# Kernel tuning notes

Hardware: AMD Instinct MI355X
Metric: run time of the kernel (lower is better)

## Reference

```python
import jax, jax.numpy as jnp
import numpy as np

N = 50000          # nodes in homogeneous graph
E_RAND = 450000    # non-self edges
R = 5              # 4 relations + identity
C = 2              # num_channels
L = 2              # num_layers
IN_DIM = 256
HID = 128
NUM_CLASS = 16
N_CAT = 10000


def setup_inputs() -> dict:
    key = jax.random.key(0)
    ks = jax.random.split(key, 10)
    h = jax.random.normal(ks[0], (N, IN_DIM), dtype=jnp.float32)
    src_r = jax.random.randint(ks[1], (E_RAND,), 0, N, dtype=jnp.int32)
    dst_r = jax.random.randint(ks[2], (E_RAND,), 0, N, dtype=jnp.int32)
    et_r = jax.random.randint(ks[3], (E_RAND,), 0, R - 1, dtype=jnp.int32)
    self_idx = jnp.arange(N, dtype=jnp.int32)
    src = jnp.concatenate([src_r, self_idx])
    dst = jnp.concatenate([dst_r, self_idx])
    etype = jnp.concatenate([et_r, jnp.full((N,), R - 1, dtype=jnp.int32)])
    category_idx = jax.random.randint(ks[4], (N_CAT,), 0, N, dtype=jnp.int32)
    # learned params
    gt_w = 0.01 * jax.random.normal(ks[5], (L, C, R), dtype=jnp.float32)
    Wc = jax.random.normal(ks[6], (C, IN_DIM, HID), dtype=jnp.float32) / np.sqrt(IN_DIM)
    W1 = jax.random.normal(ks[7], (C * HID, HID), dtype=jnp.float32) / np.sqrt(C * HID)
    b1 = jnp.zeros((HID,), dtype=jnp.float32)
    W2 = jax.random.normal(ks[8], (HID, NUM_CLASS), dtype=jnp.float32) / np.sqrt(HID)
    b2 = jnp.zeros((NUM_CLASS,), dtype=jnp.float32)
    return {"h": h, "src": src, "dst": dst, "etype": etype,
            "category_idx": category_idx, "gt_w": gt_w, "Wc": Wc,
            "W1": W1, "b1": b1, "W2": W2, "b2": b2}


def reference(h, src, dst, etype, category_idx, gt_w, Wc, W1, b1, W2, b2):
    n = h.shape[0]
    # per-channel input projection: H[c] = h @ Wc[c]  -> [C, N, HID]
    H = jnp.einsum('nd,cdh->cnh', h, Wc)
    seg = lambda v: jax.ops.segment_sum(v, dst, num_segments=n)
    for l in range(gt_w.shape[0]):
        # GTConv: per-channel softmax over relations; summed weighted adjacency
        Filt = jax.nn.softmax(gt_w[l], axis=1)        # [C, R]
        w = Filt[:, etype]                            # [C, E] edge weights
        # EdgeWeightNorm('right'): divide by weighted in-degree of dst
        deg = jax.vmap(seg)(w)                        # [C, N]
        wn = w / deg[:, dst]                          # [C, E]
        # GCNConv: sum_{e: dst=v} H[src(e)] * wn(e)
        msg = H[:, src, :] * wn[:, :, None]           # [C, E, HID]
        H = jax.vmap(seg)(msg)                        # [C, N, HID]
    # concat channels along feature dim (torch.cat(H, dim=1))
    X = jnp.transpose(H, (1, 0, 2)).reshape(n, -1)    # [N, C*HID]
    X = jax.nn.relu(X @ W1 + b1)
    y = X @ W2 + b2
    return y[category_idx]
```

## Files before the change

kernel.cpp:

```cpp
#include <hip/hip_runtime.h>
#include <hip/hip_bf16.h>

#define IN_DIM 256
#define HID 128
#define CCH 2
#define RR 5
#define LL 2
#define NCLS 16

typedef __attribute__((ext_vector_type(8))) short short8;
typedef __attribute__((ext_vector_type(4))) short short4_;
typedef __attribute__((ext_vector_type(4))) float floatx4;

__device__ __forceinline__ unsigned short f2bf(float f) {
    unsigned int u = __float_as_uint(f);
    unsigned int r = (u + 0x7FFFu + ((u >> 16) & 1u)) >> 16;
    return (unsigned short)r;
}

__global__ void cvt_weights(const float* __restrict__ Wc, const float* __restrict__ W1,
                            const float* __restrict__ gt_w,
                            unsigned short* __restrict__ WcT, unsigned short* __restrict__ W1T,
                            float* __restrict__ filt) {
    int i = blockIdx.x * 256 + threadIdx.x;
    if (blockIdx.x == 0 && threadIdx.x < LL * CCH) {
        const float* g = gt_w + threadIdx.x * RR;
        float m = -1e30f;
        for (int r = 0; r < RR; ++r) m = fmaxf(m, g[r]);
        float e[RR], s = 0.f;
        for (int r = 0; r < RR; ++r) { e[r] = __expf(g[r] - m); s += e[r]; }
        for (int r = 0; r < RR; ++r) filt[threadIdx.x * RR + r] = e[r] / s;
    }
    if (i < CCH * HID * IN_DIM) {
        int c = i >> 15;
        int rem = i & 32767;
        int d = rem >> 8;
        int k = rem & 255;
        WcT[i] = f2bf(Wc[((size_t)c * IN_DIM + k) * HID + d]);
    }
    if (i < HID * IN_DIM) {
        int d = i >> 8;
        int k = i & 255;
        W1T[i] = f2bf(W1[(size_t)k * HID + d]);
    }
}

__global__ __launch_bounds__(256, 2) void proj_mfma(const float* __restrict__ h,
                                                    const unsigned short* __restrict__ WcT,
                                                    unsigned short* __restrict__ H0, int N) {
    __shared__ unsigned short Bl[64 * 256];
    int t = threadIdx.x;
    int wv = t >> 6, l = t & 63;
    int l15 = l & 15, lq = l >> 4;
    int n0 = blockIdx.x * 64;

#pragma unroll
    for (int i = 0; i < 16; ++i) {
        int fi = t * 4 + i * 1024;
        int r = fi >> 8;
        int k = fi & 255;
        int node = n0 + r;
        const float* src = h + (size_t)(node < N ? node : N - 1) * IN_DIM + k;
        floatx4 f = *(const floatx4*)src;
        short4_ s4;
        s4[0] = (short)f2bf(f[0]); s4[1] = (short)f2bf(f[1]);
        s4[2] = (short)f2bf(f[2]); s4[3] = (short)f2bf(f[3]);
        int c = k >> 3;
        int half = (k >> 2) & 1;
        int cs = c ^ ((r & 7) << 2);
        *(short4_*)(&Bl[r * 256 + cs * 8 + half * 4]) = s4;
    }
    __syncthreads();

    floatx4 acc[4][4];
#pragma unroll
    for (int m = 0; m < 4; ++m)
#pragma unroll
        for (int n = 0; n < 4; ++n) acc[m][n] = (floatx4){0.f, 0.f, 0.f, 0.f};

#pragma unroll
    for (int kh = 0; kh < 2; ++kh) {
        short8 a[4][4];
#pragma unroll
        for (int mt0 = 0; mt0 < 4; ++mt0) {
            const unsigned short* arow = WcT + (size_t)((wv * 4 + mt0) * 16 + l15) * IN_DIM;
#pragma unroll
            for (int kk = 0; kk < 4; ++kk)
                a[mt0][kk] = *(const short8*)(arow + (kh * 4 + kk) * 32 + lq * 8);
        }
#pragma unroll
        for (int nf = 0; nf < 4; ++nf) {
            int r = nf * 16 + l15;
            short8 b[4];
#pragma unroll
            for (int kk = 0; kk < 4; ++kk) {
                int c = (kh * 4 + kk) * 4 + lq;
                int cs = c ^ ((r & 7) << 2);
                b[kk] = *(const short8*)(&Bl[r * 256 + cs * 8]);
            }
#pragma unroll
            for (int mt0 = 0; mt0 < 4; ++mt0)
#pragma unroll
                for (int kk = 0; kk < 4; ++kk)
                    acc[mt0][nf] = __builtin_amdgcn_mfma_f32_16x16x32_bf16(a[mt0][kk], b[kk],
                                                                           acc[mt0][nf], 0, 0, 0);
        }
    }

#pragma unroll
    for (int mt0 = 0; mt0 < 4; ++mt0) {
        int m0 = (wv * 4 + mt0) * 16 + lq * 4;
#pragma unroll
        for (int nf = 0; nf < 4; ++nf) {
            int node = n0 + nf * 16 + l15;
            if (node < N) {
                short4_ st;
                st[0] = (short)f2bf(acc[mt0][nf][0]); st[1] = (short)f2bf(acc[mt0][nf][1]);
                st[2] = (short)f2bf(acc[mt0][nf][2]); st[3] = (short)f2bf(acc[mt0][nf][3]);
                *(short4_*)(H0 + (size_t)node * (CCH * HID) + m0) = st;
            }
        }
    }
}

__global__ void count_kernel(const int* __restrict__ dst, int* __restrict__ counts, int E) {
    for (int e = blockIdx.x * blockDim.x + threadIdx.x; e < E; e += gridDim.x * blockDim.x)
        atomicAdd(&counts[dst[e]], 1);
}

__global__ void scanA_kernel(const int* __restrict__ counts, int* __restrict__ partials, int n) {
    __shared__ int s[256];
    int t = threadIdx.x;
    int i = blockIdx.x * 256 + t;
    int v = (i < n) ? counts[i] : 0;
    s[t] = v;
    __syncthreads();
    for (int off = 1; off < 256; off <<= 1) {
        int tv = (t >= off) ? s[t - off] : 0;
        __syncthreads();
        s[t] += tv;
        __syncthreads();
    }
    if (t == 255) partials[blockIdx.x] = s[255];
}

__global__ void scanB_kernel(const int* __restrict__ partials, int* __restrict__ chunk_off, int nchunk) {
    __shared__ int s[256];
    int t = threadIdx.x;
    int v = (t < nchunk) ? partials[t] : 0;
    s[t] = v;
    __syncthreads();
    for (int off = 1; off < 256; off <<= 1) {
        int tv = (t >= off) ? s[t - off] : 0;
        __syncthreads();
        s[t] += tv;
        __syncthreads();
    }
    if (t < nchunk) chunk_off[t] = s[t] - v;
}

__global__ void scanC_kernel(const int* __restrict__ counts, const int* __restrict__ chunk_off,
                             int* __restrict__ offsets, int* __restrict__ cursor, int n) {
    __shared__ int s[256];
    int t = threadIdx.x;
    int i = blockIdx.x * 256 + t;
    int v = (i < n) ? counts[i] : 0;
    s[t] = v;
    __syncthreads();
    for (int off = 1; off < 256; off <<= 1) {
        int tv = (t >= off) ? s[t - off] : 0;
        __syncthreads();
        s[t] += tv;
        __syncthreads();
    }
    if (i < n) {
        int incl = chunk_off[blockIdx.x] + s[t];
        offsets[i + 1] = incl;
        cursor[i] = incl - v;
    }
    if (i == 0) offsets[0] = 0;
}

__global__ void fill_kernel(const int* __restrict__ src, const int* __restrict__ dst,
                            const int* __restrict__ etype, int* __restrict__ cursor,
                            int2* __restrict__ epack, int E) {
    for (int e = blockIdx.x * blockDim.x + threadIdx.x; e < E; e += gridDim.x * blockDim.x) {
        int d = dst[e];
        int p = atomicAdd(&cursor[d], 1);
        epack[p] = make_int2(src[e], etype[e]);
    }
}

__global__ __launch_bounds__(256) void agg_kernel(const uint4* __restrict__ Hin,
                                                  uint4* __restrict__ Hout,
                                                  const int* __restrict__ offs,
                                                  const int2* __restrict__ epack,
                                                  const float* __restrict__ filt, int N) {
    int node = blockIdx.x;
    int t = threadIdx.x;
    int g = t >> 5;
    int lane32 = t & 31;
    int c = lane32 >> 4;
    float f0 = filt[c * RR + 0], f1 = filt[c * RR + 1], f2 = filt[c * RR + 2];
    float f3 = filt[c * RR + 3], f4 = filt[c * RR + 4];

    int e0 = offs[node], e1 = offs[node + 1];
    float acc[8];
#pragma unroll
    for (int r = 0; r < 8; ++r) acc[r] = 0.f;
    float deg = 0.f;

    for (int j = e0 + g; j < e1; j += 8) {
        int2 pc = epack[j];
        uint4 v = Hin[(size_t)pc.x * 32 + lane32];
        int et = pc.y;
        float w = (et == 0) ? f0 : (et == 1) ? f1 : (et == 2) ? f2 : (et == 3) ? f3 : f4;
        deg += w;
        acc[0] += w * __uint_as_float(v.x << 16);
        acc[1] += w * __uint_as_float(v.x & 0xFFFF0000u);
        acc[2] += w * __uint_as_float(v.y << 16);
        acc[3] += w * __uint_as_float(v.y & 0xFFFF0000u);
        acc[4] += w * __uint_as_float(v.z << 16);
        acc[5] += w * __uint_as_float(v.z & 0xFFFF0000u);
        acc[6] += w * __uint_as_float(v.w << 16);
        acc[7] += w * __uint_as_float(v.w & 0xFFFF0000u);
    }

#pragma unroll
    for (int r = 0; r < 8; ++r) acc[r] += __shfl_xor(acc[r], 32);
    deg += __shfl_xor(deg, 32);

    __shared__ float sacc[3][8][33];
    __shared__ float sdeg[3][33];
    int wv = t >> 6;
    bool lowhalf = (t & 63) < 32;
    if (wv > 0 && lowhalf) {
#pragma unroll
        for (int r = 0; r < 8; ++r) sacc[wv - 1][r][lane32] = acc[r];
        sdeg[wv - 1][lane32] = deg;
    }
    __syncthreads();
    if (wv == 0 && lowhalf) {
#pragma unroll
        for (int k = 0; k < 3; ++k) {
#pragma unroll
            for (int r = 0; r < 8; ++r) acc[r] += sacc[k][r][lane32];
            deg += sdeg[k][lane32];
        }
        float inv = 1.f / deg;
        uint4 o;
        o.x = (unsigned int)f2bf(acc[0] * inv) | ((unsigned int)f2bf(acc[1] * inv) << 16);
        o.y = (unsigned int)f2bf(acc[2] * inv) | ((unsigned int)f2bf(acc[3] * inv) << 16);
        o.z = (unsigned int)f2bf(acc[4] * inv) | ((unsigned int)f2bf(acc[5] * inv) << 16);
        o.w = (unsigned int)f2bf(acc[6] * inv) | ((unsigned int)f2bf(acc[7] * inv) << 16);
        Hout[(size_t)node * 32 + lane32] = o;
    }
}

__global__ __launch_bounds__(256) void mlp1_mfma(const unsigned short* __restrict__ H2,
                                                 const int* __restrict__ cat,
                                                 const unsigned short* __restrict__ W1T,
                                                 const float* __restrict__ b1,
                                                 float* __restrict__ hidden, int NCAT) {
    int t = threadIdx.x;
    int wv = t >> 6, l = t & 63;
    int l15 = l & 15, lq = l >> 4;
    int i = blockIdx.x * 64 + wv * 16 + l15;
    int iclamp = i < NCAT ? i : NCAT - 1;
    int node = cat[iclamp];

    short8 bfrag[8];
    const unsigned short* xrow = H2 + (size_t)node * (CCH * HID);
#pragma unroll
    for (int kk = 0; kk < 8; ++kk)
        bfrag[kk] = *(const short8*)(xrow + kk * 32 + lq * 8);

#pragma unroll
    for (int mt = 0; mt < 8; ++mt) {
        floatx4 acc = {0.f, 0.f, 0.f, 0.f};
        const unsigned short* arow = W1T + (size_t)(mt * 16 + l15) * (CCH * HID);
#pragma unroll
        for (int kk = 0; kk < 8; ++kk) {
            short8 a = *(const short8*)(arow + kk * 32 + lq * 8);
            acc = __builtin_amdgcn_mfma_f32_16x16x32_bf16(a, bfrag[kk], acc, 0, 0, 0);
        }
        if (i < NCAT) {
            int d0 = mt * 16 + lq * 4;
            floatx4 o;
#pragma unroll
            for (int r = 0; r < 4; ++r) o[r] = fmaxf(acc[r] + b1[d0 + r], 0.f);
            *(floatx4*)(hidden + (size_t)i * HID + d0) = o;
        }
    }
}

__global__ void mlp2_kernel(const float* __restrict__ hidden, const float* __restrict__ W2,
                            const float* __restrict__ b2, float* __restrict__ out, int NCAT) {
    int idx = blockIdx.x * 256 + threadIdx.x;
    int i = idx >> 4, cls = idx & 15;
    if (i >= NCAT) return;
    const float* hrow = hidden + (size_t)i * HID;
    float acc = b2[cls];
#pragma unroll 8
    for (int j = 0; j < HID; ++j) acc += hrow[j] * W2[j * NCLS + cls];
    out[idx] = acc;
}

extern "C" void kernel_launch(void* const* d_in, const int* in_sizes, int n_in,
                              void* d_out, int out_size, void* d_ws, size_t ws_size,
                              hipStream_t stream) {
    const float* h    = (const float*)d_in[0];
    const int* src    = (const int*)d_in[1];
    const int* dst    = (const int*)d_in[2];
    const int* etype  = (const int*)d_in[3];
    const int* cat    = (const int*)d_in[4];
    const float* gt_w = (const float*)d_in[5];
    const float* Wc   = (const float*)d_in[6];
    const float* W1   = (const float*)d_in[7];
    const float* b1   = (const float*)d_in[8];
    const float* W2   = (const float*)d_in[9];
    const float* b2   = (const float*)d_in[10];
    float* out = (float*)d_out;

    const int N = in_sizes[0] / IN_DIM;
    const int E = in_sizes[1];
    const int NCAT = in_sizes[4];
    const int NCHUNK = (N + 255) / 256;

    char* p = (char*)d_ws;
    auto alloc = [&](size_t bytes) {
        char* q = p;
        p += (bytes + 255) & ~(size_t)255;
        return q;
    };
    unsigned short* HA   = (unsigned short*)alloc((size_t)N * CCH * HID * 2);
    unsigned short* HB   = (unsigned short*)alloc((size_t)N * CCH * HID * 2);
    unsigned short* WcT  = (unsigned short*)alloc((size_t)CCH * HID * IN_DIM * 2);
    unsigned short* W1T  = (unsigned short*)alloc((size_t)HID * CCH * HID * 2);
    float* hidden        = (float*)alloc((size_t)NCAT * HID * 4);
    int*   counts        = (int*)alloc((size_t)N * 4);
    int*   offsets       = (int*)alloc((size_t)(N + 1) * 4);
    int*   cursor        = (int*)alloc((size_t)N * 4);
    int*   partials      = (int*)alloc((size_t)NCHUNK * 4);
    int*   chunk_off     = (int*)alloc((size_t)NCHUNK * 4);
    int2*  epack         = (int2*)alloc((size_t)E * 8);
    float* filt          = (float*)alloc((size_t)LL * CCH * RR * 4);

    hipMemsetAsync(counts, 0, (size_t)N * 4, stream);

    cvt_weights<<<(CCH * HID * IN_DIM + 255) / 256, 256, 0, stream>>>(Wc, W1, gt_w, WcT, W1T, filt);
    proj_mfma<<<(N + 63) / 64, 256, 0, stream>>>(h, WcT, HA, N);

    count_kernel<<<512, 256, 0, stream>>>(dst, counts, E);
    scanA_kernel<<<NCHUNK, 256, 0, stream>>>(counts, partials, N);
    scanB_kernel<<<1, 256, 0, stream>>>(partials, chunk_off, NCHUNK);
    scanC_kernel<<<NCHUNK, 256, 0, stream>>>(counts, chunk_off, offsets, cursor, N);
    fill_kernel<<<512, 256, 0, stream>>>(src, dst, etype, cursor, epack, E);

    agg_kernel<<<N, 256, 0, stream>>>((const uint4*)HA, (uint4*)HB,
                                      offsets, epack, filt, N);
    agg_kernel<<<N, 256, 0, stream>>>((const uint4*)HB, (uint4*)HA,
                                      offsets, epack, filt + CCH * RR, N);

    mlp1_mfma<<<(NCAT + 63) / 64, 256, 0, stream>>>(HA, cat, W1T, b1, hidden, NCAT);
    mlp2_kernel<<<(NCAT * NCLS + 255) / 256, 256, 0, stream>>>(hidden, W2, b2, out, NCAT);
}
```

Before: 321.1 us.

## Assign one 32-lane group per node in aggregation with software-pipelined gathers

```diff
diff --git a/kernel.cpp b/kernel.cpp
--- a/kernel.cpp
+++ b/kernel.cpp
@@ -196,10 +196,11 @@
                                                   const int* __restrict__ offs,
                                                   const int2* __restrict__ epack,
                                                   const float* __restrict__ filt, int N) {
-    int node = blockIdx.x;
     int t = threadIdx.x;
     int g = t >> 5;
     int lane32 = t & 31;
+    int node = blockIdx.x * 8 + g;
+    if (node >= N) return;
     int c = lane32 >> 4;
     float f0 = filt[c * RR + 0], f1 = filt[c * RR + 1], f2 = filt[c * RR + 2];
     float f3 = filt[c * RR + 3], f4 = filt[c * RR + 4];
@@ -210,51 +211,38 @@
     for (int r = 0; r < 8; ++r) acc[r] = 0.f;
     float deg = 0.f;
 
-    for (int j = e0 + g; j < e1; j += 8) {
-        int2 pc = epack[j];
-        uint4 v = Hin[(size_t)pc.x * 32 + lane32];
-        int et = pc.y;
-        float w = (et == 0) ? f0 : (et == 1) ? f1 : (et == 2) ? f2 : (et == 3) ? f3 : f4;
+    int2 pc = epack[e0];
+    uint4 v = Hin[(size_t)pc.x * 32 + lane32];
+    int et = pc.y;
+    for (int j = e0 + 1; ; ++j) {
+        uint4 vc = v;
+        int etc = et;
+        bool more = j < e1;
+        if (more) {
+            int2 pn = epack[j];
+            v = Hin[(size_t)pn.x * 32 + lane32];
+            et = pn.y;
+        }
+        float w = (etc == 0) ? f0 : (etc == 1) ? f1 : (etc == 2) ? f2 : (etc == 3) ? f3 : f4;
         deg += w;
-        acc[0] += w * __uint_as_float(v.x << 16);
-        acc[1] += w * __uint_as_float(v.x & 0xFFFF0000u);
-        acc[2] += w * __uint_as_float(v.y << 16);
-        acc[3] += w * __uint_as_float(v.y & 0xFFFF0000u);
-        acc[4] += w * __uint_as_float(v.z << 16);
-        acc[5] += w * __uint_as_float(v.z & 0xFFFF0000u);
-        acc[6] += w * __uint_as_float(v.w << 16);
-        acc[7] += w * __uint_as_float(v.w & 0xFFFF0000u);
-    }
-
-#pragma unroll
-    for (int r = 0; r < 8; ++r) acc[r] += __shfl_xor(acc[r], 32);
-    deg += __shfl_xor(deg, 32);
-
-    __shared__ float sacc[3][8][33];
-    __shared__ float sdeg[3][33];
-    int wv = t >> 6;
-    bool lowhalf = (t & 63) < 32;
-    if (wv > 0 && lowhalf) {
-#pragma unroll
-        for (int r = 0; r < 8; ++r) sacc[wv - 1][r][lane32] = acc[r];
-        sdeg[wv - 1][lane32] = deg;
-    }
-    __syncthreads();
-    if (wv == 0 && lowhalf) {
-#pragma unroll
-        for (int k = 0; k < 3; ++k) {
-#pragma unroll
-            for (int r = 0; r < 8; ++r) acc[r] += sacc[k][r][lane32];
-            deg += sdeg[k][lane32];
-        }
-        float inv = 1.f / deg;
-        uint4 o;
-        o.x = (unsigned int)f2bf(acc[0] * inv) | ((unsigned int)f2bf(acc[1] * inv) << 16);
-        o.y = (unsigned int)f2bf(acc[2] * inv) | ((unsigned int)f2bf(acc[3] * inv) << 16);
-        o.z = (unsigned int)f2bf(acc[4] * inv) | ((unsigned int)f2bf(acc[5] * inv) << 16);
-        o.w = (unsigned int)f2bf(acc[6] * inv) | ((unsigned int)f2bf(acc[7] * inv) << 16);
-        Hout[(size_t)node * 32 + lane32] = o;
-    }
+        acc[0] += w * __uint_as_float(vc.x << 16);
+        acc[1] += w * __uint_as_float(vc.x & 0xFFFF0000u);
+        acc[2] += w * __uint_as_float(vc.y << 16);
+        acc[3] += w * __uint_as_float(vc.y & 0xFFFF0000u);
+        acc[4] += w * __uint_as_float(vc.z << 16);
+        acc[5] += w * __uint_as_float(vc.z & 0xFFFF0000u);
+        acc[6] += w * __uint_as_float(vc.w << 16);
+        acc[7] += w * __uint_as_float(vc.w & 0xFFFF0000u);
+        if (!more) break;
+    }
+
+    float inv = 1.f / deg;
+    uint4 o;
+    o.x = (unsigned int)f2bf(acc[0] * inv) | ((unsigned int)f2bf(acc[1] * inv) << 16);
+    o.y = (unsigned int)f2bf(acc[2] * inv) | ((unsigned int)f2bf(acc[3] * inv) << 16);
+    o.z = (unsigned int)f2bf(acc[4] * inv) | ((unsigned int)f2bf(acc[5] * inv) << 16);
+    o.w = (unsigned int)f2bf(acc[6] * inv) | ((unsigned int)f2bf(acc[7] * inv) << 16);
+    Hout[(size_t)node * 32 + lane32] = o;
 }
 
 __global__ __launch_bounds__(256) void mlp1_mfma(const unsigned short* __restrict__ H2,
@@ -357,10 +345,10 @@
     scanC_kernel<<<NCHUNK, 256, 0, stream>>>(counts, chunk_off, offsets, cursor, N);
     fill_kernel<<<512, 256, 0, stream>>>(src, dst, etype, cursor, epack, E);
 
-    agg_kernel<<<N, 256, 0, stream>>>((const uint4*)HA, (uint4*)HB,
-                                      offsets, epack, filt, N);
-    agg_kernel<<<N, 256, 0, stream>>>((const uint4*)HB, (uint4*)HA,
-                                      offsets, epack, filt + CCH * RR, N);
+    agg_kernel<<<(N + 7) / 8, 256, 0, stream>>>((const uint4*)HA, (uint4*)HB,
+                                                offsets, epack, filt, N);
+    agg_kernel<<<(N + 7) / 8, 256, 0, stream>>>((const uint4*)HB, (uint4*)HA,
+                                                offsets, epack, filt + CCH * RR, N);
 
     mlp1_mfma<<<(NCAT + 63) / 64, 256, 0, stream>>>(HA, cat, W1T, b1, hidden, NCAT);
     mlp2_kernel<<<(NCAT * NCLS + 255) / 256, 256, 0, stream>>>(hidden, W2, b2, out, NCAT);
```

Result: faster. 296.7 us (-7.6%).
